# Kernel tuning notes

Measured on AMD Instinct MI355X. Metric: run time of the kernel, lower is better.

Reference implementation:

```python
import jax, jax.numpy as jnp
import numpy as np

N, D, DIN, S, R = 128, 2560, 5120, 16, 160  # users, d_model, d_inner, d_state, dt_rank


def setup_inputs() -> dict:
    key = jax.random.key(0)
    ks = jax.random.split(key, 16)
    f = lambda k, shape, s: jax.random.normal(k, shape, dtype=jnp.float32) * s
    return {
        "x": f(ks[0], (1, 1, N, D), 1.0),
        "conv_state0": f(ks[1], (1, 1, N, DIN), 0.1),
        "conv_state1": f(ks[2], (1, 1, N, DIN), 0.1),
        "conv_state2": f(ks[3], (1, 1, N, DIN), 0.1),
        "conv_state3": f(ks[4], (1, 1, N, DIN), 0.1),
        "ssm_state": f(ks[5], (N, DIN, S), 0.1),
        "ssm_proj": f(ks[6], (D, DIN), 0.02),
        "mlp_proj": f(ks[7], (D, DIN), 0.02),
        "down_proj": f(ks[8], (DIN, D), 0.02),
        "conv_w": f(ks[9], (4, DIN), 0.2),
        "conv_bias": f(ks[10], (DIN,), 0.1),
        "x_proj_w": f(ks[11], (DIN, R + 2 * S), 0.02),
        "dt_proj_w": f(ks[12], (R, DIN), 0.05),
        "dt_proj_b": f(ks[13], (DIN,), 0.1),
        "A_log": jnp.log(jnp.broadcast_to(jnp.arange(1, S + 1, dtype=jnp.float32), (DIN, S))),
        "D_param": jnp.ones((DIN,), jnp.float32),
    }


def reference(x, conv_state0, conv_state1, conv_state2, conv_state3, ssm_state,
              ssm_proj, mlp_proj, down_proj, conv_w, conv_bias,
              x_proj_w, dt_proj_w, dt_proj_b, A_log, D_param):
    r = dt_proj_w.shape[0]
    s = A_log.shape[1]
    x2 = x[0, 0]                         # (N, D)
    xs = x2 @ ssm_proj                   # (N, DIN) in_proj (ssm half)
    # shifted conv state window: oldest state (conv_state0) is dropped
    states = (conv_state1[0, 0], conv_state2[0, 0], conv_state3[0, 0], xs)
    conv_out = conv_bias + conv_w[0] * states[0] + conv_w[1] * states[1] \
        + conv_w[2] * states[2] + conv_w[3] * states[3]   # (N, DIN)
    u = jax.nn.silu(conv_out)
    # selective-scan single step (TtMambaSSM)
    proj = u @ x_proj_w                  # (N, R + 2S)
    dt = jax.nn.softplus(proj[:, :r] @ dt_proj_w + dt_proj_b)  # (N, DIN)
    Bm = proj[:, r:r + s]                # (N, S)
    Cm = proj[:, r + s:]                 # (N, S)
    A = -jnp.exp(A_log)                  # (DIN, S)
    dA = jnp.exp(dt[:, :, None] * A[None])                     # (N, DIN, S)
    h = dA * ssm_state + dt[:, :, None] * Bm[:, None, :] * u[:, :, None]
    y = jnp.einsum('nds,ns->nd', h, Cm) + D_param * u          # (N, DIN)
    # residual/gate branch and output projection (note: no silu on res, as in source)
    res = x2 @ mlp_proj                  # (N, DIN)
    out = (y * res) @ down_proj          # (N, D)
    return out[None, None]               # (1, 1, N, D)
```

## Files before the change

### kernel.cpp

```cpp
#include <hip/hip_runtime.h>

using u16 = unsigned short;
using u32 = unsigned int;

typedef __attribute__((ext_vector_type(8))) short short8;
typedef __attribute__((ext_vector_type(4))) float floatx4;

constexpr int TOKENS = 128;
constexpr int DM = 2560;
constexpr int DI = 5120;
constexpr int NS = 16;
constexpr int NR = 160;
constexpr int NP = 192;

constexpr size_t XS_OFF   = 0;
constexpr size_t RES_OFF  = XS_OFF  + (size_t)TOKENS * DI;
constexpr size_t U_OFF    = RES_OFF + (size_t)TOKENS * DI;
constexpr size_t DT_OFF   = U_OFF   + (size_t)TOKENS * DI;
constexpr size_t PROJ_OFF = DT_OFF  + (size_t)TOKENS * DI;
constexpr size_t OACC_OFF = PROJ_OFF + (size_t)TOKENS * NP;

__device__ __forceinline__ float bf2f(u16 h) {
  u32 u = ((u32)h) << 16;
  return __builtin_bit_cast(float, u);
}
__device__ __forceinline__ u16 f2bf(float f) {
  u32 u = __builtin_bit_cast(u32, f);
  u += 0x7FFFu + ((u >> 16) & 1u);
  return (u16)(u >> 16);
}
__device__ __forceinline__ u32 pk2(float a, float b) {
  u32 r;
  asm("v_cvt_pk_bf16_f32 %0, %1, %2" : "=v"(r) : "v"(a), "v"(b));
  return r;
}
__device__ __forceinline__ float ldsc(const void* p, size_t i, bool bf) {
  return bf ? bf2f(((const u16*)p)[i]) : ((const float*)p)[i];
}
__device__ __forceinline__ uint4 ld8(const void* p, size_t i, bool bf) {
  if (bf) return *(const uint4*)((const u16*)p + i);
  const float4* f = (const float4*)((const float*)p + i);
  float4 a = f[0], b = f[1];
  return (uint4){pk2(a.x, a.y), pk2(a.z, a.w), pk2(b.x, b.y), pk2(b.z, b.w)};
}
__device__ __forceinline__ void ld8f(const void* p, size_t i, bool bf, float* o) {
  if (bf) {
    uint4 v = *(const uint4*)((const u16*)p + i);
    const u16* h = (const u16*)&v;
#pragma unroll
    for (int e = 0; e < 8; e++) o[e] = bf2f(h[e]);
  } else {
    const float4* f = (const float4*)((const float*)p + i);
    float4 a = f[0], b = f[1];
    o[0] = a.x; o[1] = a.y; o[2] = a.z; o[3] = a.w;
    o[4] = b.x; o[5] = b.y; o[6] = b.z; o[7] = b.w;
  }
}

struct GemmP {
  const void* A; int lda; int a_ws;
  const void* B; const void* B2;
  float* C; float* C2;
  int ldb; int ldc;
  int ksteps;
  int nx_half;
  int atomic;
  const u32* probe;
};

template <int BK>
__global__ __launch_bounds__(256, 4) void gemm_t(GemmP p) {
  constexpr int NBLK = BK / 8;
  constexpr int MASK = NBLK - 1;
  constexpr int KK = BK / 32;
  constexpr int LOGN = (BK == 64) ? 3 : 2;
  constexpr int RP = 256 / NBLK;
  constexpr int PA = 128 / RP;

  __shared__ __align__(16) u16 As[128 * BK];
  __shared__ __align__(16) u16 Bs[64 * BK];

  const bool bf = (p.probe[0] != 0u);
  const int tid = threadIdx.x;
  const int bx = blockIdx.x;
  const void* B = p.B; float* C = p.C;
  int nblk = bx;
  if (bx >= p.nx_half) { B = p.B2; C = p.C2; nblk = bx - p.nx_half; }
  const int n0 = nblk * 64;
  const int kstart = blockIdx.y * p.ksteps * BK;

  const int wave = tid >> 6, lane = tid & 63;
  const int q = lane >> 4, l16 = lane & 15;
  const int wx = wave & 1, wy = wave >> 1;

  const bool a_f32 = p.a_ws || !bf;

  const int ac = tid & MASK;
  const int am0 = tid >> LOGN;
  const int bc = tid & 7;
  const int br = tid >> 3;
  const int bn8 = bc * 8;

  floatx4 acc[4][2];
#pragma unroll
  for (int mi = 0; mi < 4; mi++)
#pragma unroll
    for (int ni = 0; ni < 2; ni++) acc[mi][ni] = (floatx4){0.f, 0.f, 0.f, 0.f};

  auto load_tiles = [&](int ks, uint4* aO, uint4* bO) {
    const int kb = kstart + ks * BK;
#pragma unroll
    for (int pa = 0; pa < PA; pa++) {
      const int m = am0 + pa * RP;
      const size_t off = (size_t)m * p.lda + kb + ac * 8;
      if (!a_f32) {
        aO[pa] = *(const uint4*)((const u16*)p.A + off);
      } else {
        const float4* f = (const float4*)((const float*)p.A + off);
        float4 x0 = f[0], x1 = f[1];
        aO[pa] = (uint4){pk2(x0.x, x0.y), pk2(x0.z, x0.w),
                         pk2(x1.x, x1.y), pk2(x1.z, x1.w)};
      }
    }
    if constexpr (BK == 64) {
      bO[0] = ld8(B, (size_t)(kb + 2 * br) * p.ldb + n0 + bn8, bf);
      bO[1] = ld8(B, (size_t)(kb + 2 * br + 1) * p.ldb + n0 + bn8, bf);
    } else {
      bO[0] = ld8(B, (size_t)(kb + br) * p.ldb + n0 + bn8, bf);
    }
  };

  auto store_tiles = [&](const uint4* aO, const uint4* bO) {
#pragma unroll
    for (int pa = 0; pa < PA; pa++) {
      const int m = am0 + pa * RP;
      *(uint4*)&As[m * BK + ((ac ^ (m & MASK)) << 3)] = aO[pa];
    }
    if constexpr (BK == 64) {
      const u16* lo = (const u16*)&bO[0];
      const u16* hi = (const u16*)&bO[1];
      const int k2 = 2 * br;
#pragma unroll
      for (int j = 0; j < 8; j++) {
        const int n = bn8 + j;
        const int blk = (k2 >> 3) ^ ((n ^ (n >> 3)) & MASK);
        *(u32*)&Bs[n * BK + (blk << 3) + (k2 & 7)] =
            (u32)lo[j] | ((u32)hi[j] << 16);
      }
    } else {
      const u16* lo = (const u16*)&bO[0];
#pragma unroll
      for (int j = 0; j < 8; j++) {
        const int n = bn8 + j;
        const int blk = (br >> 3) ^ ((n ^ (n >> 3)) & MASK);
        Bs[n * BK + (blk << 3) + (br & 7)] = lo[j];
      }
    }
  };

  const int swA = l16 & MASK;
  const int arow = (wy * 64 + l16) * BK;
  int nrow[2], swb[2];
#pragma unroll
  for (int ni = 0; ni < 2; ni++) {
    const int n = wx * 32 + ni * 16 + l16;
    nrow[ni] = n * BK;
    swb[ni] = (n ^ (n >> 3)) & MASK;
  }

  auto compute = [&]() {
#pragma unroll
    for (int kk = 0; kk < KK; kk++) {
      const int kq = kk * 4 + q;
      const int ao = (kq ^ swA) << 3;
      short8 a[4];
#pragma unroll
      for (int mi = 0; mi < 4; mi++)
        a[mi] = __builtin_bit_cast(short8,
            *(const uint4*)&As[arow + mi * 16 * BK + ao]);
      short8 b[2];
#pragma unroll
      for (int ni = 0; ni < 2; ni++)
        b[ni] = __builtin_bit_cast(short8,
            *(const uint4*)&Bs[nrow[ni] + ((kq ^ swb[ni]) << 3)]);
#pragma unroll
      for (int mi = 0; mi < 4; mi++)
#pragma unroll
        for (int ni = 0; ni < 2; ni++)
          acc[mi][ni] = __builtin_amdgcn_mfma_f32_16x16x32_bf16(
              a[mi], b[ni], acc[mi][ni], 0, 0, 0);
    }
  };

  uint4 a0[PA], b0[KK], a1[PA], b1[KK];
  load_tiles(0, a0, b0);
  if (p.ksteps > 1) load_tiles(1, a1, b1);
  int ks = 0;
  for (;;) {
    __syncthreads();
    store_tiles(a0, b0);
    if (ks + 2 < p.ksteps) load_tiles(ks + 2, a0, b0);
    __syncthreads();
    compute();
    if (++ks == p.ksteps) break;

    __syncthreads();
    store_tiles(a1, b1);
    if (ks + 2 < p.ksteps) load_tiles(ks + 2, a1, b1);
    __syncthreads();
    compute();
    if (++ks == p.ksteps) break;
  }

  if (p.atomic) {
#pragma unroll
    for (int ni = 0; ni < 2; ni++) {
      const int col = n0 + wx * 32 + ni * 16 + l16;
#pragma unroll
      for (int mi = 0; mi < 4; mi++) {
        floatx4 v = acc[mi][ni];
#pragma unroll
        for (int r = 0; r < 4; r++) {
          const int row = wy * 64 + mi * 16 + q * 4 + r;
          atomicAdd(&C[(size_t)row * p.ldc + col], v[r]);
        }
      }
    }
  } else {
#pragma unroll
    for (int ni = 0; ni < 2; ni++) {
      const int col = n0 + wx * 32 + ni * 16 + l16;
#pragma unroll
      for (int mi = 0; mi < 4; mi++) {
        floatx4 v = acc[mi][ni];
#pragma unroll
        for (int r = 0; r < 4; r++) {
          const int row = wy * 64 + mi * 16 + q * 4 + r;
          C[(size_t)row * p.ldc + col] = v[r];
        }
      }
    }
  }
}

__global__ __launch_bounds__(256) void epi_u_k(
    const float* __restrict__ xs_acc, const void* __restrict__ cs1,
    const void* __restrict__ cs2, const void* __restrict__ cs3,
    const void* __restrict__ cw, const void* __restrict__ cb,
    float* __restrict__ u, const u32* __restrict__ probe) {
  const bool bf = (probe[0] != 0u);
  const int idx = blockIdx.x * 256 + threadIdx.x;
  const int n = idx / (DI / 8);
  const int d0 = (idx - n * (DI / 8)) * 8;
  const size_t nd = (size_t)n * DI + d0;
  float xv[8];
  {
    const float4* f = (const float4*)(xs_acc + nd);
    float4 a = f[0], b = f[1];
    xv[0] = a.x; xv[1] = a.y; xv[2] = a.z; xv[3] = a.w;
    xv[4] = b.x; xv[5] = b.y; xv[6] = b.z; xv[7] = b.w;
  }
  float c1[8], c2[8], c3[8], w0[8], w1[8], w2[8], w3[8], bb[8];
  ld8f(cs1, nd, bf, c1);
  ld8f(cs2, nd, bf, c2);
  ld8f(cs3, nd, bf, c3);
  ld8f(cw, (size_t)0 * DI + d0, bf, w0);
  ld8f(cw, (size_t)1 * DI + d0, bf, w1);
  ld8f(cw, (size_t)2 * DI + d0, bf, w2);
  ld8f(cw, (size_t)3 * DI + d0, bf, w3);
  ld8f(cb, d0, bf, bb);
  float o[8];
#pragma unroll
  for (int e = 0; e < 8; e++) {
    float cv = bb[e] + w0[e] * c1[e] + w1[e] * c2[e] + w2[e] * c3[e] +
               w3[e] * xv[e];
    o[e] = cv / (1.0f + __expf(-cv));
  }
  float4* uo = (float4*)(u + nd);
  uo[0] = (float4){o[0], o[1], o[2], o[3]};
  uo[1] = (float4){o[4], o[5], o[6], o[7]};
}

__global__ __launch_bounds__(256) void ssm_k(
    const void* __restrict__ sstate, const void* __restrict__ alog,
    const void* __restrict__ dparam, const void* __restrict__ dtb,
    const float* __restrict__ proj, const float* __restrict__ dtacc,
    const float* __restrict__ u, const float* __restrict__ res,
    float* __restrict__ z, const u32* __restrict__ probe) {
  const bool bf = (probe[0] != 0u);
  const int n = blockIdx.y;
  const int d = blockIdx.x * 256 + threadIdx.x;
  __shared__ float Bsh[NS], Csh[NS];
  if (threadIdx.x < NS)
    Bsh[threadIdx.x] = proj[(size_t)n * NP + NR + threadIdx.x];
  else if (threadIdx.x < 2 * NS)
    Csh[threadIdx.x - NS] = proj[(size_t)n * NP + NR + threadIdx.x];
  __syncthreads();
  const size_t nd = (size_t)n * DI + d;
  const float uv = u[nd], rv = res[nd];
  float sv = dtacc[nd] + ldsc(dtb, d, bf);
  const float dtv = (sv > 20.0f) ? sv : log1pf(__expf(sv));

  float stf[16], alf[16];
  if (bf) {
    u16 st[16], al[16];
    const uint4* sp = (const uint4*)((const u16*)sstate + nd * 16);
    *(uint4*)&st[0] = sp[0]; *(uint4*)&st[8] = sp[1];
    const uint4* ap = (const uint4*)((const u16*)alog + (size_t)d * 16);
    *(uint4*)&al[0] = ap[0]; *(uint4*)&al[8] = ap[1];
#pragma unroll
    for (int s = 0; s < 16; s++) { stf[s] = bf2f(st[s]); alf[s] = bf2f(al[s]); }
  } else {
    const float4* sp = (const float4*)((const float*)sstate + nd * 16);
    const float4* ap = (const float4*)((const float*)alog + (size_t)d * 16);
#pragma unroll
    for (int i = 0; i < 4; i++) {
      float4 s4 = sp[i], a4 = ap[i];
      stf[i * 4 + 0] = s4.x; stf[i * 4 + 1] = s4.y; stf[i * 4 + 2] = s4.z; stf[i * 4 + 3] = s4.w;
      alf[i * 4 + 0] = a4.x; alf[i * 4 + 1] = a4.y; alf[i * 4 + 2] = a4.z; alf[i * 4 + 3] = a4.w;
    }
  }
  float y = 0.f;
#pragma unroll
  for (int s = 0; s < 16; s++) {
    float Aa = -__expf(alf[s]);
    float dA = __expf(dtv * Aa);
    float h = dA * stf[s] + dtv * Bsh[s] * uv;
    y += h * Csh[s];
  }
  y += ldsc(dparam, d, bf) * uv;
  z[nd] = y * rv;
}

__global__ __launch_bounds__(256) void cvt_k(const float* __restrict__ in,
                                             void* __restrict__ out, int n,
                                             const u32* __restrict__ probe) {
  const bool bf = (probe[0] != 0u);
  const int i0 = (blockIdx.x * 256 + threadIdx.x) * 8;
  if (i0 + 8 <= n) {
    const float4* f = (const float4*)(in + i0);
    float4 a = f[0], b = f[1];
    if (bf) {
      uint4 v = {pk2(a.x, a.y), pk2(a.z, a.w), pk2(b.x, b.y), pk2(b.z, b.w)};
      *(uint4*)((u16*)out + i0) = v;
    } else {
      float4* o = (float4*)((float*)out + i0);
      o[0] = a; o[1] = b;
    }
  } else {
    for (int i = i0; i < n; i++) {
      if (bf) ((u16*)out)[i] = f2bf(in[i]);
      else    ((float*)out)[i] = in[i];
    }
  }
}

extern "C" void kernel_launch(void* const* d_in, const int* in_sizes, int n_in,
                              void* d_out, int out_size, void* d_ws, size_t ws_size,
                              hipStream_t stream) {
  const void* x         = d_in[0];
  const void* cs1       = d_in[2];
  const void* cs2       = d_in[3];
  const void* cs3       = d_in[4];
  const void* ssm_state = d_in[5];
  const void* ssm_proj  = d_in[6];
  const void* mlp_proj  = d_in[7];
  const void* down_proj = d_in[8];
  const void* conv_w    = d_in[9];
  const void* conv_b    = d_in[10];
  const void* x_proj_w  = d_in[11];
  const void* dt_proj_w = d_in[12];
  const void* dt_proj_b = d_in[13];
  const void* A_log     = d_in[14];
  const void* D_param   = d_in[15];
  const u32*  probe     = (const u32*)A_log;

  float* ws     = (float*)d_ws;
  float* xs_acc = ws + XS_OFF;
  float* z      = ws + XS_OFF;
  float* res    = ws + RES_OFF;
  float* u      = ws + U_OFF;
  float* dtacc  = ws + DT_OFF;
  float* proj   = ws + PROJ_OFF;
  float* oacc   = ws + OACC_OFF;

  hipMemsetAsync(xs_acc, 0, (size_t)TOKENS * DI * sizeof(float), stream);
  hipMemsetAsync(res,    0, (size_t)TOKENS * DI * sizeof(float), stream);
  hipMemsetAsync(dtacc,  0, (size_t)TOKENS * DI * sizeof(float), stream);
  hipMemsetAsync(proj,   0, (size_t)TOKENS * NP * sizeof(float), stream);
  hipMemsetAsync(oacc,   0, (size_t)TOKENS * DM * sizeof(float), stream);

  {
    GemmP p{};
    p.A = x; p.lda = DM; p.a_ws = 0;
    p.B = ssm_proj; p.B2 = mlp_proj;
    p.C = xs_acc; p.C2 = res;
    p.ldb = DI; p.ldc = DI;
    p.ksteps = 5; p.nx_half = 80; p.atomic = 1;
    p.probe = probe;
    gemm_t<64><<<dim3(160, 8), 256, 0, stream>>>(p);
  }
  epi_u_k<<<dim3(TOKENS * DI / 8 / 256), 256, 0, stream>>>(
      xs_acc, cs1, cs2, cs3, conv_w, conv_b, u, probe);
  {
    GemmP p{};
    p.A = u; p.lda = DI; p.a_ws = 1;
    p.B = x_proj_w; p.B2 = nullptr;
    p.C = proj; p.C2 = nullptr;
    p.ldb = NP; p.ldc = NP;
    p.ksteps = 1; p.nx_half = 1 << 30; p.atomic = 1;
    p.probe = probe;
    gemm_t<64><<<dim3(3, 80), 256, 0, stream>>>(p);
  }
  {
    GemmP p{};
    p.A = proj; p.lda = NP; p.a_ws = 1;
    p.B = dt_proj_w; p.B2 = nullptr;
    p.C = dtacc; p.C2 = nullptr;
    p.ldb = DI; p.ldc = DI;
    p.ksteps = 1; p.nx_half = 1 << 30; p.atomic = 1;
    p.probe = probe;
    gemm_t<32><<<dim3(DI / 64, 5), 256, 0, stream>>>(p);
  }
  ssm_k<<<dim3(DI / 256, TOKENS), 256, 0, stream>>>(
      ssm_state, A_log, D_param, dt_proj_b, proj, dtacc, u, res, z, probe);
  {
    GemmP p{};
    p.A = z; p.lda = DI; p.a_ws = 1;
    p.B = down_proj; p.B2 = nullptr;
    p.C = oacc; p.C2 = nullptr;
    p.ldb = DM; p.ldc = DM;
    p.ksteps = 5; p.nx_half = 1 << 30; p.atomic = 1;
    p.probe = probe;
    gemm_t<64><<<dim3(DM / 64, 16), 256, 0, stream>>>(p);
  }
  cvt_k<<<dim3((out_size / 8 + 255) / 256), 256, 0, stream>>>(oacc, d_out, out_size, probe);
}
```

Baseline: 336.0 us.

## Replace atomic split-K accumulation with per-slice partial buffers reduced in consumers

When the workspace is large enough, each split-K GEMM slice writes its partial tile with plain stores into its own buffer. The following elementwise kernels (conv epilogue, a new proj reduction, ssm, output convert) sum the slices as they read them. This drops the memsets and the contention of float atomics. The GEMM is also unified to a single BK=32 tile with fewer threads loading B, and the code falls back to the atomic path when workspace is small. The cost is much more workspace and extra reads of partial buffers (8x for xs/res, 16x for the output) in the consumer kernels.

```diff
diff --git a/kernel.cpp b/kernel.cpp
--- a/kernel.cpp
+++ b/kernel.cpp
@@ -13,12 +13,21 @@
 constexpr int NR = 160;
 constexpr int NP = 192;
 
-constexpr size_t XS_OFF   = 0;
-constexpr size_t RES_OFF  = XS_OFF  + (size_t)TOKENS * DI;
-constexpr size_t U_OFF    = RES_OFF + (size_t)TOKENS * DI;
-constexpr size_t DT_OFF   = U_OFF   + (size_t)TOKENS * DI;
-constexpr size_t PROJ_OFF = DT_OFF  + (size_t)TOKENS * DI;
-constexpr size_t OACC_OFF = PROJ_OFF + (size_t)TOKENS * NP;
+constexpr size_t ND    = (size_t)TOKENS * DI;
+constexpr size_t XS_P  = 0;
+constexpr size_t RES_P = XS_P + 8 * ND;
+constexpr size_t U_OFF = RES_P + 8 * ND;
+constexpr size_t DT_P  = U_OFF + ND;
+constexpr size_t PRJ_P = DT_P + 5 * ND;
+constexpr size_t PRJ   = PRJ_P + 40 * (size_t)(TOKENS * NP);
+constexpr size_t NEED  = PRJ + (size_t)(TOKENS * NP);
+
+constexpr size_t S_XS  = 0;
+constexpr size_t S_RES = S_XS + ND;
+constexpr size_t S_U   = S_RES + ND;
+constexpr size_t S_DT  = S_U + ND;
+constexpr size_t S_PRJ = S_DT + ND;
+constexpr size_t S_OAC = S_PRJ + (size_t)(TOKENS * NP);
 
 __device__ __forceinline__ float bf2f(u16 h) {
   u32 u = ((u32)h) << 16;
@@ -65,20 +74,13 @@
   int ksteps;
   int nx_half;
   int atomic;
+  size_t cstride;
   const u32* probe;
 };
 
-template <int BK>
-__global__ __launch_bounds__(256, 4) void gemm_t(GemmP p) {
-  constexpr int NBLK = BK / 8;
-  constexpr int MASK = NBLK - 1;
-  constexpr int KK = BK / 32;
-  constexpr int LOGN = (BK == 64) ? 3 : 2;
-  constexpr int RP = 256 / NBLK;
-  constexpr int PA = 128 / RP;
-
-  __shared__ __align__(16) u16 As[128 * BK];
-  __shared__ __align__(16) u16 Bs[64 * BK];
+__global__ __launch_bounds__(256, 4) void gemm_k(GemmP p) {
+  __shared__ __align__(16) u16 As[128 * 32];
+  __shared__ __align__(16) u16 Bs[64 * 32];
 
   const bool bf = (p.probe[0] != 0u);
   const int tid = threadIdx.x;
@@ -87,7 +89,8 @@
   int nblk = bx;
   if (bx >= p.nx_half) { B = p.B2; C = p.C2; nblk = bx - p.nx_half; }
   const int n0 = nblk * 64;
-  const int kstart = blockIdx.y * p.ksteps * BK;
+  const int kstart = blockIdx.y * p.ksteps * 32;
+  if (!p.atomic) C += blockIdx.y * p.cstride;
 
   const int wave = tid >> 6, lane = tid & 63;
   const int q = lane >> 4, l16 = lane & 15;
@@ -95,11 +98,11 @@
 
   const bool a_f32 = p.a_ws || !bf;
 
-  const int ac = tid & MASK;
-  const int am0 = tid >> LOGN;
-  const int bc = tid & 7;
-  const int br = tid >> 3;
-  const int bn8 = bc * 8;
+  const int ac = tid & 3;
+  const int am0 = tid >> 2;
+  const bool bact = tid < 128;
+  const int bc = tid & 7, pr = (tid >> 3) & 15;
+  const int bn8 = bc * 8, k2 = 2 * pr;
 
   floatx4 acc[4][2];
 #pragma unroll
@@ -108,10 +111,10 @@
     for (int ni = 0; ni < 2; ni++) acc[mi][ni] = (floatx4){0.f, 0.f, 0.f, 0.f};
 
   auto load_tiles = [&](int ks, uint4* aO, uint4* bO) {
-    const int kb = kstart + ks * BK;
-#pragma unroll
-    for (int pa = 0; pa < PA; pa++) {
-      const int m = am0 + pa * RP;
+    const int kb = kstart + ks * 32;
+#pragma unroll
+    for (int pa = 0; pa < 2; pa++) {
+      const int m = am0 + pa * 64;
       const size_t off = (size_t)m * p.lda + kb + ac * 8;
       if (!a_f32) {
         aO[pa] = *(const uint4*)((const u16*)p.A + off);
@@ -122,77 +125,61 @@
                          pk2(x1.x, x1.y), pk2(x1.z, x1.w)};
       }
     }
-    if constexpr (BK == 64) {
-      bO[0] = ld8(B, (size_t)(kb + 2 * br) * p.ldb + n0 + bn8, bf);
-      bO[1] = ld8(B, (size_t)(kb + 2 * br + 1) * p.ldb + n0 + bn8, bf);
-    } else {
-      bO[0] = ld8(B, (size_t)(kb + br) * p.ldb + n0 + bn8, bf);
+    if (bact) {
+      bO[0] = ld8(B, (size_t)(kb + k2) * p.ldb + n0 + bn8, bf);
+      bO[1] = ld8(B, (size_t)(kb + k2 + 1) * p.ldb + n0 + bn8, bf);
     }
   };
 
   auto store_tiles = [&](const uint4* aO, const uint4* bO) {
 #pragma unroll
-    for (int pa = 0; pa < PA; pa++) {
-      const int m = am0 + pa * RP;
-      *(uint4*)&As[m * BK + ((ac ^ (m & MASK)) << 3)] = aO[pa];
-    }
-    if constexpr (BK == 64) {
+    for (int pa = 0; pa < 2; pa++) {
+      const int m = am0 + pa * 64;
+      *(uint4*)&As[m * 32 + ((ac ^ (m & 3)) << 3)] = aO[pa];
+    }
+    if (bact) {
       const u16* lo = (const u16*)&bO[0];
       const u16* hi = (const u16*)&bO[1];
-      const int k2 = 2 * br;
 #pragma unroll
       for (int j = 0; j < 8; j++) {
         const int n = bn8 + j;
-        const int blk = (k2 >> 3) ^ ((n ^ (n >> 3)) & MASK);
-        *(u32*)&Bs[n * BK + (blk << 3) + (k2 & 7)] =
+        const int blk = (k2 >> 3) ^ ((n ^ (n >> 3)) & 3);
+        *(u32*)&Bs[n * 32 + (blk << 3) + (k2 & 7)] =
             (u32)lo[j] | ((u32)hi[j] << 16);
       }
-    } else {
-      const u16* lo = (const u16*)&bO[0];
-#pragma unroll
-      for (int j = 0; j < 8; j++) {
-        const int n = bn8 + j;
-        const int blk = (br >> 3) ^ ((n ^ (n >> 3)) & MASK);
-        Bs[n * BK + (blk << 3) + (br & 7)] = lo[j];
-      }
     }
   };
 
-  const int swA = l16 & MASK;
-  const int arow = (wy * 64 + l16) * BK;
-  int nrow[2], swb[2];
+  const int swA = l16 & 3;
+  const int arow = (wy * 64 + l16) * 32;
+  const int ao = ((q ^ swA) << 3);
+  int nrow[2], bo[2];
 #pragma unroll
   for (int ni = 0; ni < 2; ni++) {
     const int n = wx * 32 + ni * 16 + l16;
-    nrow[ni] = n * BK;
-    swb[ni] = (n ^ (n >> 3)) & MASK;
+    nrow[ni] = n * 32;
+    bo[ni] = ((q ^ ((n ^ (n >> 3)) & 3)) << 3);
   }
 
   auto compute = [&]() {
-#pragma unroll
-    for (int kk = 0; kk < KK; kk++) {
-      const int kq = kk * 4 + q;
-      const int ao = (kq ^ swA) << 3;
-      short8 a[4];
-#pragma unroll
-      for (int mi = 0; mi < 4; mi++)
-        a[mi] = __builtin_bit_cast(short8,
-            *(const uint4*)&As[arow + mi * 16 * BK + ao]);
-      short8 b[2];
+    short8 a[4];
+#pragma unroll
+    for (int mi = 0; mi < 4; mi++)
+      a[mi] = __builtin_bit_cast(short8,
+          *(const uint4*)&As[arow + mi * 16 * 32 + ao]);
+    short8 b[2];
+#pragma unroll
+    for (int ni = 0; ni < 2; ni++)
+      b[ni] = __builtin_bit_cast(short8, *(const uint4*)&Bs[nrow[ni] + bo[ni]]);
+#pragma unroll
+    for (int mi = 0; mi < 4; mi++)
 #pragma unroll
       for (int ni = 0; ni < 2; ni++)
-        b[ni] = __builtin_bit_cast(short8,
-            *(const uint4*)&Bs[nrow[ni] + ((kq ^ swb[ni]) << 3)]);
-#pragma unroll
-      for (int mi = 0; mi < 4; mi++)
-#pragma unroll
-        for (int ni = 0; ni < 2; ni++)
-          acc[mi][ni] = __builtin_amdgcn_mfma_f32_16x16x32_bf16(
-              a[mi], b[ni], acc[mi][ni], 0, 0, 0);
-    }
+        acc[mi][ni] = __builtin_amdgcn_mfma_f32_16x16x32_bf16(
+            a[mi], b[ni], acc[mi][ni], 0, 0, 0);
   };
 
-  uint4 a0[PA], b0[KK], a1[PA], b1[KK];
+  uint4 a0[2], b0[2], a1[2], b1[2];
   load_tiles(0, a0, b0);
   if (p.ksteps > 1) load_tiles(1, a1, b1);
   int ks = 0;
@@ -212,53 +199,39 @@
     if (++ks == p.ksteps) break;
   }
 
-  if (p.atomic) {
-#pragma unroll
-    for (int ni = 0; ni < 2; ni++) {
-      const int col = n0 + wx * 32 + ni * 16 + l16;
-#pragma unroll
-      for (int mi = 0; mi < 4; mi++) {
-        floatx4 v = acc[mi][ni];
-#pragma unroll
-        for (int r = 0; r < 4; r++) {
-          const int row = wy * 64 + mi * 16 + q * 4 + r;
-          atomicAdd(&C[(size_t)row * p.ldc + col], v[r]);
-        }
+#pragma unroll
+  for (int ni = 0; ni < 2; ni++) {
+    const int col = n0 + wx * 32 + ni * 16 + l16;
+#pragma unroll
+    for (int mi = 0; mi < 4; mi++) {
+      floatx4 v = acc[mi][ni];
+#pragma unroll
+      for (int r = 0; r < 4; r++) {
+        const int row = wy * 64 + mi * 16 + q * 4 + r;
+        if (p.atomic) atomicAdd(&C[(size_t)row * p.ldc + col], v[r]);
+        else          C[(size_t)row * p.ldc + col] = v[r];
       }
     }
-  } else {
-#pragma unroll
-    for (int ni = 0; ni < 2; ni++) {
-      const int col = n0 + wx * 32 + ni * 16 + l16;
-#pragma unroll
-      for (int mi = 0; mi < 4; mi++) {
-        floatx4 v = acc[mi][ni];
-#pragma unroll
-        for (int r = 0; r < 4; r++) {
-          const int row = wy * 64 + mi * 16 + q * 4 + r;
-          C[(size_t)row * p.ldc + col] = v[r];
-        }
-      }
-    }
   }
 }
 
 __global__ __launch_bounds__(256) void epi_u_k(
-    const float* __restrict__ xs_acc, const void* __restrict__ cs1,
-    const void* __restrict__ cs2, const void* __restrict__ cs3,
-    const void* __restrict__ cw, const void* __restrict__ cb,
-    float* __restrict__ u, const u32* __restrict__ probe) {
+    const float* __restrict__ xs_p, int nred, size_t pstride,
+    const void* __restrict__ cs1, const void* __restrict__ cs2,
+    const void* __restrict__ cs3, const void* __restrict__ cw,
+    const void* __restrict__ cb, float* __restrict__ u,
+    const u32* __restrict__ probe) {
   const bool bf = (probe[0] != 0u);
   const int idx = blockIdx.x * 256 + threadIdx.x;
   const int n = idx / (DI / 8);
   const int d0 = (idx - n * (DI / 8)) * 8;
   const size_t nd = (size_t)n * DI + d0;
-  float xv[8];
-  {
-    const float4* f = (const float4*)(xs_acc + nd);
+  float xv[8] = {0.f, 0.f, 0.f, 0.f, 0.f, 0.f, 0.f, 0.f};
+  for (int j = 0; j < nred; j++) {
+    const float4* f = (const float4*)(xs_p + j * pstride + nd);
     float4 a = f[0], b = f[1];
-    xv[0] = a.x; xv[1] = a.y; xv[2] = a.z; xv[3] = a.w;
-    xv[4] = b.x; xv[5] = b.y; xv[6] = b.z; xv[7] = b.w;
+    xv[0] += a.x; xv[1] += a.y; xv[2] += a.z; xv[3] += a.w;
+    xv[4] += b.x; xv[5] += b.y; xv[6] += b.z; xv[7] += b.w;
   }
   float c1[8], c2[8], c3[8], w0[8], w1[8], w2[8], w3[8], bb[8];
   ld8f(cs1, nd, bf, c1);
@@ -281,11 +254,23 @@
   uo[1] = (float4){o[4], o[5], o[6], o[7]};
 }
 
+__global__ __launch_bounds__(256) void rproj_k(const float* __restrict__ in,
+                                               int nred, size_t pstride,
+                                               float* __restrict__ out) {
+  const int i = blockIdx.x * 256 + threadIdx.x;
+  if (i < TOKENS * NP) {
+    float s = 0.f;
+    for (int j = 0; j < nred; j++) s += in[j * pstride + i];
+    out[i] = s;
+  }
+}
+
 __global__ __launch_bounds__(256) void ssm_k(
     const void* __restrict__ sstate, const void* __restrict__ alog,
     const void* __restrict__ dparam, const void* __restrict__ dtb,
-    const float* __restrict__ proj, const float* __restrict__ dtacc,
-    const float* __restrict__ u, const float* __restrict__ res,
+    const float* __restrict__ proj, const float* __restrict__ dt_p,
+    int nred_d, size_t sd, const float* __restrict__ u,
+    const float* __restrict__ res_p, int nred_r, size_t sr,
     float* __restrict__ z, const u32* __restrict__ probe) {
   const bool bf = (probe[0] != 0u);
   const int n = blockIdx.y;
@@ -297,8 +282,11 @@
     Csh[threadIdx.x - NS] = proj[(size_t)n * NP + NR + threadIdx.x];
   __syncthreads();
   const size_t nd = (size_t)n * DI + d;
-  const float uv = u[nd], rv = res[nd];
-  float sv = dtacc[nd] + ldsc(dtb, d, bf);
+  const float uv = u[nd];
+  float rv = 0.f;
+  for (int j = 0; j < nred_r; j++) rv += res_p[j * sr + nd];
+  float sv = ldsc(dtb, d, bf);
+  for (int j = 0; j < nred_d; j++) sv += dt_p[j * sd + nd];
   const float dtv = (sv > 20.0f) ? sv : log1pf(__expf(sv));
 
   float stf[16], alf[16];
@@ -333,24 +321,33 @@
 }
 
 __global__ __launch_bounds__(256) void cvt_k(const float* __restrict__ in,
+                                             int nred, size_t pstride,
                                              void* __restrict__ out, int n,
                                              const u32* __restrict__ probe) {
   const bool bf = (probe[0] != 0u);
   const int i0 = (blockIdx.x * 256 + threadIdx.x) * 8;
   if (i0 + 8 <= n) {
-    const float4* f = (const float4*)(in + i0);
-    float4 a = f[0], b = f[1];
+    float o[8] = {0.f, 0.f, 0.f, 0.f, 0.f, 0.f, 0.f, 0.f};
+    for (int j = 0; j < nred; j++) {
+      const float4* f = (const float4*)(in + j * pstride + i0);
+      float4 a = f[0], b = f[1];
+      o[0] += a.x; o[1] += a.y; o[2] += a.z; o[3] += a.w;
+      o[4] += b.x; o[5] += b.y; o[6] += b.z; o[7] += b.w;
+    }
     if (bf) {
-      uint4 v = {pk2(a.x, a.y), pk2(a.z, a.w), pk2(b.x, b.y), pk2(b.z, b.w)};
+      uint4 v = {pk2(o[0], o[1]), pk2(o[2], o[3]), pk2(o[4], o[5]), pk2(o[6], o[7])};
       *(uint4*)((u16*)out + i0) = v;
     } else {
-      float4* o = (float4*)((float*)out + i0);
-      o[0] = a; o[1] = b;
+      float4* fo = (float4*)((float*)out + i0);
+      fo[0] = (float4){o[0], o[1], o[2], o[3]};
+      fo[1] = (float4){o[4], o[5], o[6], o[7]};
     }
   } else {
     for (int i = i0; i < n; i++) {
-      if (bf) ((u16*)out)[i] = f2bf(in[i]);
-      else    ((float*)out)[i] = in[i];
+      float s = 0.f;
+      for (int j = 0; j < nred; j++) s += in[j * pstride + i];
+      if (bf) ((u16*)out)[i] = f2bf(s);
+      else    ((float*)out)[i] = s;
     }
   }
 }
@@ -375,64 +372,131 @@
   const void* D_param   = d_in[15];
   const u32*  probe     = (const u32*)A_log;
 
-  float* ws     = (float*)d_ws;
-  float* xs_acc = ws + XS_OFF;
-  float* z      = ws + XS_OFF;
-  float* res    = ws + RES_OFF;
-  float* u      = ws + U_OFF;
-  float* dtacc  = ws + DT_OFF;
-  float* proj   = ws + PROJ_OFF;
-  float* oacc   = ws + OACC_OFF;
-
-  hipMemsetAsync(xs_acc, 0, (size_t)TOKENS * DI * sizeof(float), stream);
-  hipMemsetAsync(res,    0, (size_t)TOKENS * DI * sizeof(float), stream);
-  hipMemsetAsync(dtacc,  0, (size_t)TOKENS * DI * sizeof(float), stream);
-  hipMemsetAsync(proj,   0, (size_t)TOKENS * NP * sizeof(float), stream);
-  hipMemsetAsync(oacc,   0, (size_t)TOKENS * DM * sizeof(float), stream);
-
-  {
-    GemmP p{};
-    p.A = x; p.lda = DM; p.a_ws = 0;
-    p.B = ssm_proj; p.B2 = mlp_proj;
-    p.C = xs_acc; p.C2 = res;
-    p.ldb = DI; p.ldc = DI;
-    p.ksteps = 5; p.nx_half = 80; p.atomic = 1;
-    p.probe = probe;
-    gemm_t<64><<<dim3(160, 8), 256, 0, stream>>>(p);
-  }
-  epi_u_k<<<dim3(TOKENS * DI / 8 / 256), 256, 0, stream>>>(
-      xs_acc, cs1, cs2, cs3, conv_w, conv_b, u, probe);
-  {
-    GemmP p{};
-    p.A = u; p.lda = DI; p.a_ws = 1;
-    p.B = x_proj_w; p.B2 = nullptr;
-    p.C = proj; p.C2 = nullptr;
-    p.ldb = NP; p.ldc = NP;
-    p.ksteps = 1; p.nx_half = 1 << 30; p.atomic = 1;
-    p.probe = probe;
-    gemm_t<64><<<dim3(3, 80), 256, 0, stream>>>(p);
-  }
-  {
-    GemmP p{};
-    p.A = proj; p.lda = NP; p.a_ws = 1;
-    p.B = dt_proj_w; p.B2 = nullptr;
-    p.C = dtacc; p.C2 = nullptr;
-    p.ldb = DI; p.ldc = DI;
-    p.ksteps = 1; p.nx_half = 1 << 30; p.atomic = 1;
-    p.probe = probe;
-    gemm_t<32><<<dim3(DI / 64, 5), 256, 0, stream>>>(p);
-  }
-  ssm_k<<<dim3(DI / 256, TOKENS), 256, 0, stream>>>(
-      ssm_state, A_log, D_param, dt_proj_b, proj, dtacc, u, res, z, probe);
-  {
-    GemmP p{};
-    p.A = z; p.lda = DI; p.a_ws = 1;
-    p.B = down_proj; p.B2 = nullptr;
-    p.C = oacc; p.C2 = nullptr;
-    p.ldb = DM; p.ldc = DM;
-    p.ksteps = 5; p.nx_half = 1 << 30; p.atomic = 1;
-    p.probe = probe;
-    gemm_t<64><<<dim3(DM / 64, 16), 256, 0, stream>>>(p);
-  }
-  cvt_k<<<dim3((out_size / 8 + 255) / 256), 256, 0, stream>>>(oacc, d_out, out_size, probe);
-}
+  float* ws = (float*)d_ws;
+  const bool big = (ws_size / sizeof(float)) >= NEED;
+
+  if (big) {
+    float* xs_p  = ws + XS_P;
+    float* res_p = ws + RES_P;
+    float* u     = ws + U_OFF;
+    float* dt_p  = ws + DT_P;
+    float* prj_p = ws + PRJ_P;
+    float* prj   = ws + PRJ;
+    float* z     = ws + XS_P;
+    float* oac_p = ws + RES_P;
+
+    {
+      GemmP p{};
+      p.A = x; p.lda = DM; p.a_ws = 0;
+      p.B = ssm_proj; p.B2 = mlp_proj;
+      p.C = xs_p; p.C2 = res_p;
+      p.ldb = DI; p.ldc = DI;
+      p.ksteps = 10; p.nx_half = 80; p.atomic = 0; p.cstride = ND;
+      p.probe = probe;
+      gemm_k<<<dim3(160, 8), 256, 0, stream>>>(p);
+    }
+    epi_u_k<<<dim3(TOKENS * DI / 8 / 256), 256, 0, stream>>>(
+        xs_p, 8, ND, cs1, cs2, cs3, conv_w, conv_b, u, probe);
+    {
+      GemmP p{};
+      p.A = u; p.lda = DI; p.a_ws = 1;
+      p.B = x_proj_w; p.B2 = nullptr;
+      p.C = prj_p; p.C2 = nullptr;
+      p.ldb = NP; p.ldc = NP;
+      p.ksteps = 4; p.nx_half = 1 << 30; p.atomic = 0;
+      p.cstride = (size_t)TOKENS * NP;
+      p.probe = probe;
+      gemm_k<<<dim3(3, 40), 256, 0, stream>>>(p);
+    }
+    rproj_k<<<dim3((TOKENS * NP + 255) / 256), 256, 0, stream>>>(
+        prj_p, 40, (size_t)TOKENS * NP, prj);
+    {
+      GemmP p{};
+      p.A = prj; p.lda = NP; p.a_ws = 1;
+      p.B = dt_proj_w; p.B2 = nullptr;
+      p.C = dt_p; p.C2 = nullptr;
+      p.ldb = DI; p.ldc = DI;
+      p.ksteps = 1; p.nx_half = 1 << 30; p.atomic = 0; p.cstride = ND;
+      p.probe = probe;
+      gemm_k<<<dim3(DI / 64, 5), 256, 0, stream>>>(p);
+    }
+    ssm_k<<<dim3(DI / 256, TOKENS), 256, 0, stream>>>(
+        ssm_state, A_log, D_param, dt_proj_b, prj, dt_p, 5, ND, u,
+        res_p, 8, ND, z, probe);
+    {
+      GemmP p{};
+      p.A = z; p.lda = DI; p.a_ws = 1;
+      p.B = down_proj; p.B2 = nullptr;
+      p.C = oac_p; p.C2 = nullptr;
+      p.ldb = DM; p.ldc = DM;
+      p.ksteps = 10; p.nx_half = 1 << 30; p.atomic = 0;
+      p.cstride = (size_t)TOKENS * DM;
+      p.probe = probe;
+      gemm_k<<<dim3(DM / 64, 16), 256, 0, stream>>>(p);
+    }
+    cvt_k<<<dim3((out_size / 8 + 255) / 256), 256, 0, stream>>>(
+        oac_p, 16, (size_t)TOKENS * DM, d_out, out_size, probe);
+  } else {
+    float* xs  = ws + S_XS;
+    float* res = ws + S_RES;
+    float* u   = ws + S_U;
+    float* dt  = ws + S_DT;
+    float* prj = ws + S_PRJ;
+    float* oac = ws + S_OAC;
+    float* z   = ws + S_XS;
+
+    hipMemsetAsync(xs,  0, ND * sizeof(float), stream);
+    hipMemsetAsync(res, 0, ND * sizeof(float), stream);
+    hipMemsetAsync(dt,  0, ND * sizeof(float), stream);
+    hipMemsetAsync(prj, 0, (size_t)TOKENS * NP * sizeof(float), stream);
+    hipMemsetAsync(oac, 0, (size_t)TOKENS * DM * sizeof(float), stream);
+
+    {
+      GemmP p{};
+      p.A = x; p.lda = DM; p.a_ws = 0;
+      p.B = ssm_proj; p.B2 = mlp_proj;
+      p.C = xs; p.C2 = res;
+      p.ldb = DI; p.ldc = DI;
+      p.ksteps = 10; p.nx_half = 80; p.atomic = 1; p.cstride = 0;
+      p.probe = probe;
+      gemm_k<<<dim3(160, 8), 256, 0, stream>>>(p);
+    }
+    epi_u_k<<<dim3(TOKENS * DI / 8 / 256), 256, 0, stream>>>(
+        xs, 1, 0, cs1, cs2, cs3, conv_w, conv_b, u, probe);
+    {
+      GemmP p{};
+      p.A = u; p.lda = DI; p.a_ws = 1;
+      p.B = x_proj_w; p.B2 = nullptr;
+      p.C = prj; p.C2 = nullptr;
+      p.ldb = NP; p.ldc = NP;
+      p.ksteps = 4; p.nx_half = 1 << 30; p.atomic = 1; p.cstride = 0;
+      p.probe = probe;
+      gemm_k<<<dim3(3, 40), 256, 0, stream>>>(p);
+    }
+    {
+      GemmP p{};
+      p.A = prj; p.lda = NP; p.a_ws = 1;
+      p.B = dt_proj_w; p.B2 = nullptr;
+      p.C = dt; p.C2 = nullptr;
+      p.ldb = DI; p.ldc = DI;
+      p.ksteps = 1; p.nx_half = 1 << 30; p.atomic = 1; p.cstride = 0;
+      p.probe = probe;
+      gemm_k<<<dim3(DI / 64, 5), 256, 0, stream>>>(p);
+    }
+    ssm_k<<<dim3(DI / 256, TOKENS), 256, 0, stream>>>(
+        ssm_state, A_log, D_param, dt_proj_b, prj, dt, 1, 0, u,
+        res, 1, 0, z, probe);
+    {
+      GemmP p{};
+      p.A = z; p.lda = DI; p.a_ws = 1;
+      p.B = down_proj; p.B2 = nullptr;
+      p.C = oac; p.C2 = nullptr;
+      p.ldb = DM; p.ldc = DM;
+      p.ksteps = 10; p.nx_half = 1 << 30; p.atomic = 1; p.cstride = 0;
+      p.probe = probe;
+      gemm_k<<<dim3(DM / 64, 16), 256, 0, stream>>>(p);
+    }
+    cvt_k<<<dim3((out_size / 8 + 255) / 256), 256, 0, stream>>>(
+        oac, 1, 0, d_out, out_size, probe);
+  }
+}
```

After: 340.5 us. About the same (+1.3%).
